# Kernel tuning notes

Measured on AMD Instinct MI355X. Metric: run time of the kernel, lower is better.

Reference implementation:

```python
import jax, jax.numpy as jnp
import numpy as np

B, C, H, W = 4, 8, 384, 384
CHANS = 18  # MLP hidden width (module default chans=18)
BAND = 32   # half-width of acquired low-frequency band


def setup_inputs() -> dict:
    key = jax.random.key(0)
    ks = jax.random.split(key, 8)
    acquired_kspace = jax.random.normal(ks[0], (B, C, H, W, 2), jnp.float32)
    acquiring_kspace = jax.random.normal(ks[1], (B, C, H, W, 2), jnp.float32)
    mid = W // 2
    am = np.zeros((B, W), np.float32)
    am[:, mid - BAND:mid + BAND] = 1.0  # acquired center band -> left/right well-defined
    acquired_mask = jnp.asarray(am)
    qm = np.zeros((B, W), np.float32)
    qm[:, ::24] = 1.0  # columns currently being acquired
    acquiring_mask = jnp.asarray(qm)
    CH = C * H
    IN = 2 * CH  # concat(acquiring_features, acquired_features)
    # MLP: Linear(IN,CHANS)+ReLU, Linear(CHANS,CHANS)+ReLU x2, Linear(CHANS,1)+Sigmoid (pools=4 layers)
    W1 = jax.random.normal(ks[2], (CHANS, IN), jnp.float32) * 0.02
    b1 = jnp.zeros((CHANS,), jnp.float32)
    W2 = jax.random.normal(ks[3], (CHANS, CHANS), jnp.float32) * 0.02
    b2 = jnp.zeros((CHANS,), jnp.float32)
    W3 = jax.random.normal(ks[4], (CHANS, CHANS), jnp.float32) * 0.02
    b3 = jnp.zeros((CHANS,), jnp.float32)
    W4 = jax.random.normal(ks[5], (1, CHANS), jnp.float32) * 0.02
    b4 = jnp.zeros((1,), jnp.float32)
    return dict(acquired_kspace=acquired_kspace, acquiring_kspace=acquiring_kspace,
                acquired_mask=acquired_mask, acquiring_mask=acquiring_mask,
                W1=W1, b1=b1, W2=W2, b2=b2, W3=W3, b3=b3, W4=W4, b4=b4)


def reference(acquired_kspace, acquiring_kspace, acquired_mask, acquiring_mask,
              W1, b1, W2, b2, W3, b3, W4, b4):
    cabs = lambda x: jnp.sqrt(jnp.sum(x * x, axis=-1))  # complex magnitude of trailing (re,im)
    # per-column flattened features, row-major over (C,H) like torch.flatten: [B, W, C*H]
    Fq = cabs(acquiring_kspace).transpose(0, 3, 1, 2).reshape(B, W, -1)
    Fa = cabs(acquired_kspace).transpose(0, 3, 1, 2).reshape(B, W, -1)
    CH = Fq.shape[-1]
    # split first linear over the concat([acquiring, acquired]) input
    Pq = Fq @ W1[:, :CH].T   # [B, W_i, CHANS]
    Pa = Fa @ W1[:, CH:].T   # [B, W_c, CHANS]
    h = jax.nn.relu(Pq[:, :, None, :] + Pa[:, None, :, :] + b1)  # [B, W_i, W_c, CHANS]
    h = jax.nn.relu(h @ W2.T + b2)
    h = jax.nn.relu(h @ W3.T + b3)
    out = jax.nn.sigmoid(h @ W4.T + b4)[..., 0]  # [B, W_i, W_c]
    # faithful left/right bounds from acquired_mask (same as torch.nonzero(...)[0][0])
    mid = W // 2
    right = mid + jnp.argmax(acquired_mask[:, mid:] < 1.0, axis=1)              # [B]
    left = jnp.argmax(acquired_mask[:, :mid][:, ::-1] < 1.0, axis=1) + 1        # [B]
    c = jnp.arange(W)
    cmask = (c[None, :] >= left[:, None]) & (c[None, :] < right[:, None])       # [B, W_c]
    denom = (right - left).astype(out.dtype)
    heat = jnp.sum(out * cmask[:, None, :].astype(out.dtype), axis=2) / denom[:, None]
    heat = jnp.where(acquiring_mask > 0, heat, jnp.zeros_like(heat))            # only nonzero acquiring cols
    return jnp.broadcast_to(heat[:, None, :], (B, H, W))  # torch.cat of h copies along dim=1
```

## Files before the change

### kernel.cpp

```cpp
#include <hip/hip_runtime.h>
#include <math.h>
#include <limits.h>

#define kB 4
#define kC 8
#define kH 384
#define kW 384
#define kCH (kC * kH)
#define kIN (2 * kCH)
#define kNC 18
#define kMID (kW / 2)

#define NCH 8
#define RPC (kCH / NCH)
#define NGRP 48
#define kN (kB * kW * kNC)

#define E18(M) M(0) M(1) M(2) M(3) M(4) M(5) M(6) M(7) M(8) M(9) M(10) M(11) M(12) M(13) M(14) M(15) M(16) M(17)
#define E12(M) M(0) M(1) M(2) M(3) M(4) M(5) M(6) M(7) M(8) M(9) M(10) M(11)

__global__ __launch_bounds__(256)
void proj_kernel(const float* __restrict__ acquired,
                 const float* __restrict__ acquiring,
                 const float* __restrict__ am,
                 const float* __restrict__ qm,
                 const float* __restrict__ W1,
                 float* __restrict__ Pq_part, float* __restrict__ Pa_part) {
    int g = blockIdx.x, chunk = blockIdx.y, b = blockIdx.z;
    int tid = threadIdx.x;
    int w0 = g * 8;
    int r0 = chunk * RPC;

    __shared__ int sL[256], sR[256];
    __shared__ float sQm[8];
    int candR = INT_MAX, candL = INT_MAX;
    for (int i = tid; i < kW - kMID; i += 256)
        if (am[b * kW + kMID + i] < 1.0f) candR = min(candR, i);
    for (int i = tid; i < kMID; i += 256)
        if (am[b * kW + (kMID - 1 - i)] < 1.0f) candL = min(candL, i);
    sL[tid] = candL; sR[tid] = candR;
    if (tid < 8) sQm[tid] = qm[b * kW + w0 + tid];
    __syncthreads();
    for (int s = 128; s > 0; s >>= 1) {
        if (tid < s) {
            sL[tid] = min(sL[tid], sL[tid + s]);
            sR[tid] = min(sR[tid], sR[tid + s]);
        }
        __syncthreads();
    }
    int left  = ((sL[0] == INT_MAX) ? 0 : sL[0]) + 1;
    int right = kMID + ((sR[0] == INT_MAX) ? 0 : sR[0]);

    bool band = (left < w0 + 8) && (right > w0);
    bool acq_any = (sQm[0] > 0.f) || (sQm[1] > 0.f) || (sQm[2] > 0.f) || (sQm[3] > 0.f) ||
                   (sQm[4] > 0.f) || (sQm[5] > 0.f) || (sQm[6] > 0.f) || (sQm[7] > 0.f);
    if (!band && !acq_any) return;

    int c8 = tid & 7, r32 = tid >> 3;
    int w = w0 + c8;
    int lane = tid & 63, wave = tid >> 6;

    __shared__ float sW[RPC][20];
    __shared__ float sRed[4][8][kNC];

    for (int pass = 0; pass < 2; ++pass) {
        bool need = (pass == 0) ? band : acq_any;
        if (!need) continue;
        const float* ks = (pass == 0) ? acquired : acquiring;
        const float* w1 = (pass == 0) ? (W1 + kCH) : W1;

        const float* colp = ks + ((size_t)(b * kCH + r0 + r32) * kW + w) * 2;
#define KLOAD(it) const float2 v##it = *reinterpret_cast<const float2*>(colp + (size_t)(it) * 32 * kW * 2);
        E12(KLOAD)
#define KMAG(it) const float f##it = sqrtf(v##it.x * v##it.x + v##it.y * v##it.y);
        E12(KMAG)

        __syncthreads();
        for (int t = tid; t < kNC * RPC; t += 256) {
            int j = t / RPC, i = t - j * RPC;
            sW[i][j] = w1[j * kIN + r0 + i];
        }
        __syncthreads();

#define PDECL(j) float a##j = 0.0f;
        E18(PDECL)

#define ROWF(it) { \
            const float* row = &sW[r32 + 32 * (it)][0]; \
            const float4 q0 = *reinterpret_cast<const float4*>(row); \
            const float4 q1 = *reinterpret_cast<const float4*>(row + 4); \
            const float4 q2 = *reinterpret_cast<const float4*>(row + 8); \
            const float4 q3 = *reinterpret_cast<const float4*>(row + 12); \
            const float2 q4 = *reinterpret_cast<const float2*>(row + 16); \
            const float f = f##it; \
            a0  = fmaf(f, q0.x, a0);  a1  = fmaf(f, q0.y, a1);  \
            a2  = fmaf(f, q0.z, a2);  a3  = fmaf(f, q0.w, a3);  \
            a4  = fmaf(f, q1.x, a4);  a5  = fmaf(f, q1.y, a5);  \
            a6  = fmaf(f, q1.z, a6);  a7  = fmaf(f, q1.w, a7);  \
            a8  = fmaf(f, q2.x, a8);  a9  = fmaf(f, q2.y, a9);  \
            a10 = fmaf(f, q2.z, a10); a11 = fmaf(f, q2.w, a11); \
            a12 = fmaf(f, q3.x, a12); a13 = fmaf(f, q3.y, a13); \
            a14 = fmaf(f, q3.z, a14); a15 = fmaf(f, q3.w, a15); \
            a16 = fmaf(f, q4.x, a16); a17 = fmaf(f, q4.y, a17); }
        E12(ROWF)

#define WRED(j) { a##j += __shfl_down(a##j, 32, 64); a##j += __shfl_down(a##j, 16, 64); \
                  a##j += __shfl_down(a##j, 8, 64); }
        E18(WRED)
        if (lane < 8) {
#define SSTORE(j) sRed[wave][lane][j] = a##j;
            E18(SSTORE)
        }
        __syncthreads();
        if (tid < 8 * kNC) {
            int c = tid / kNC, j = tid - c * kNC;
            float s = sRed[0][c][j] + sRed[1][c][j] + sRed[2][c][j] + sRed[3][c][j];
            float* Pp = (pass == 0) ? Pa_part : Pq_part;
            Pp[((size_t)chunk * kB * kW + (size_t)b * kW + (w0 + c)) * kNC + j] = s;
        }
    }
}

__global__ __launch_bounds__(256)
void reduce_kernel(const float* __restrict__ Pa_part, const float* __restrict__ Pq_part,
                   float* __restrict__ Pa, float* __restrict__ Pq) {
    int idx = blockIdx.x * 256 + threadIdx.x;
    if (idx >= 2 * kN) return;
    const float* src = (idx < kN) ? Pa_part : Pq_part;
    float* dst = (idx < kN) ? Pa : Pq;
    int n = (idx < kN) ? idx : idx - kN;
    float s = 0.0f;
#pragma unroll
    for (int c = 0; c < NCH; ++c) s += src[(size_t)c * kN + n];
    dst[n] = s;
}

__global__ __launch_bounds__(256)
void pair_kernel(const float* __restrict__ Pq, const float* __restrict__ Pa,
                 const float* __restrict__ am, const float* __restrict__ qmask,
                 const float* __restrict__ b1, const float* __restrict__ W2,
                 const float* __restrict__ b2, const float* __restrict__ W3,
                 const float* __restrict__ b3, const float* __restrict__ W4,
                 const float* __restrict__ b4, float* __restrict__ heat) {
    int wi = blockIdx.x, b = blockIdx.y, tid = threadIdx.x;
    if (!(qmask[b * kW + wi] > 0.0f)) return;

    __shared__ int sL[256], sR[256];
    int candR = INT_MAX, candL = INT_MAX;
    for (int i = tid; i < kW - kMID; i += 256)
        if (am[b * kW + kMID + i] < 1.0f) candR = min(candR, i);
    for (int i = tid; i < kMID; i += 256)
        if (am[b * kW + (kMID - 1 - i)] < 1.0f) candL = min(candL, i);
    sL[tid] = candL; sR[tid] = candR;
    __syncthreads();
    for (int s = 128; s > 0; s >>= 1) {
        if (tid < s) {
            sL[tid] = min(sL[tid], sL[tid + s]);
            sR[tid] = min(sR[tid], sR[tid + s]);
        }
        __syncthreads();
    }
    int left  = ((sL[0] == INT_MAX) ? 0 : sL[0]) + 1;
    int right = kMID + ((sR[0] == INT_MAX) ? 0 : sR[0]);
    int span = right - left;

    __shared__ float2 sW2[kNC * kNC / 2], sW3[kNC * kNC / 2];
    __shared__ float sW4[kNC], sb1[kNC], sb2[kNC], sb3[kNC], sPq[kNC];
    __shared__ float sb4s, wred[4];
    if (tid < kNC * kNC / 2) {
        sW2[tid] = reinterpret_cast<const float2*>(W2)[tid];
        sW3[tid] = reinterpret_cast<const float2*>(W3)[tid];
    }
    if (tid >= 192 && tid < 192 + kNC) {
        int j = tid - 192;
        sPq[j] = Pq[((size_t)(b * kW + wi)) * kNC + j];
        sW4[j] = W4[j]; sb1[j] = b1[j]; sb2[j] = b2[j]; sb3[j] = b3[j];
    }
    if (tid == 255) sb4s = b4[0];
    __syncthreads();

#define DOT2(S, k, v) (S[(k)*9+0].x*v##0  + S[(k)*9+0].y*v##1  + \
                       S[(k)*9+1].x*v##2  + S[(k)*9+1].y*v##3  + \
                       S[(k)*9+2].x*v##4  + S[(k)*9+2].y*v##5  + \
                       S[(k)*9+3].x*v##6  + S[(k)*9+3].y*v##7  + \
                       S[(k)*9+4].x*v##8  + S[(k)*9+4].y*v##9  + \
                       S[(k)*9+5].x*v##10 + S[(k)*9+5].y*v##11 + \
                       S[(k)*9+6].x*v##12 + S[(k)*9+6].y*v##13 + \
                       S[(k)*9+7].x*v##14 + S[(k)*9+7].y*v##15 + \
                       S[(k)*9+8].x*v##16 + S[(k)*9+8].y*v##17)

    float ssum = 0.0f;
    for (int wc = left + tid; wc < right; wc += 256) {
        const float* pa = Pa + (size_t)(b * kW + wc) * kNC;
#define L1(j) float x##j = fmaxf(sPq[j] + sb1[j] + pa[j], 0.0f);
        E18(L1)
        asm volatile("" ::: "memory");
#define L2(k) float y##k = fmaxf(sb2[k] + DOT2(sW2, k, x), 0.0f);
        E18(L2)
        asm volatile("" ::: "memory");
#define L3(k) float z##k = fmaxf(sb3[k] + DOT2(sW3, k, y), 0.0f);
        E18(L3)
        asm volatile("" ::: "memory");
        float t = sb4s +
            (sW4[0]*z0 + sW4[1]*z1 + sW4[2]*z2 + sW4[3]*z3 + sW4[4]*z4 + sW4[5]*z5 +
             sW4[6]*z6 + sW4[7]*z7 + sW4[8]*z8 + sW4[9]*z9 + sW4[10]*z10 + sW4[11]*z11 +
             sW4[12]*z12 + sW4[13]*z13 + sW4[14]*z14 + sW4[15]*z15 + sW4[16]*z16 + sW4[17]*z17);
        ssum += 1.0f / (1.0f + expf(-t));
    }

    ssum += __shfl_down(ssum, 32, 64); ssum += __shfl_down(ssum, 16, 64);
    ssum += __shfl_down(ssum,  8, 64); ssum += __shfl_down(ssum,  4, 64);
    ssum += __shfl_down(ssum,  2, 64); ssum += __shfl_down(ssum,  1, 64);
    int wave = tid >> 6, lane = tid & 63;
    if (lane == 0) wred[wave] = ssum;
    __syncthreads();
    if (tid == 0)
        heat[b * kW + wi] = (wred[0] + wred[1] + wred[2] + wred[3]) / (float)span;
}

__global__ __launch_bounds__(256)
void out_kernel(const float* __restrict__ heat, const float* __restrict__ qm,
                float* __restrict__ out) {
    int idx = blockIdx.x * 256 + threadIdx.x;
    if (idx >= kB * kH * kW) return;
    int w = idx % kW;
    int b = idx / (kH * kW);
    out[idx] = (qm[b * kW + w] > 0.0f) ? heat[b * kW + w] : 0.0f;
}

extern "C" void kernel_launch(void* const* d_in, const int* in_sizes, int n_in,
                              void* d_out, int out_size, void* d_ws, size_t ws_size,
                              hipStream_t stream) {
    const float* acquired       = (const float*)d_in[0];
    const float* acquiring      = (const float*)d_in[1];
    const float* acquired_mask  = (const float*)d_in[2];
    const float* acquiring_mask = (const float*)d_in[3];
    const float* W1 = (const float*)d_in[4];
    const float* b1 = (const float*)d_in[5];
    const float* W2 = (const float*)d_in[6];
    const float* b2 = (const float*)d_in[7];
    const float* W3 = (const float*)d_in[8];
    const float* b3 = (const float*)d_in[9];
    const float* W4 = (const float*)d_in[10];
    const float* b4 = (const float*)d_in[11];
    float* out = (float*)d_out;

    float* Pa_part = (float*)d_ws;
    float* Pq_part = Pa_part + (size_t)NCH * kN;
    float* Pa      = Pq_part + (size_t)NCH * kN;
    float* Pq      = Pa + kN;
    float* heat    = Pq + kN;

    proj_kernel<<<dim3(NGRP, NCH, kB), 256, 0, stream>>>(
        acquired, acquiring, acquired_mask, acquiring_mask, W1, Pq_part, Pa_part);
    reduce_kernel<<<(2 * kN + 255) / 256, 256, 0, stream>>>(Pa_part, Pq_part, Pa, Pq);
    pair_kernel<<<dim3(kW, kB), 256, 0, stream>>>(
        Pq, Pa, acquired_mask, acquiring_mask,
        b1, W2, b2, W3, b3, W4, b4, heat);
    int n = kB * kH * kW;
    out_kernel<<<(n + 255) / 256, 256, 0, stream>>>(heat, acquiring_mask, out);
}
```

Before: 149.8 us.

## Fuse reduce and output kernels into proj/pair and split passes across blocks

Cuts the pipeline from four kernel launches to two. The chunk-partial reduction moves into pair_kernel, which stages the summed Pa band into shared memory. The output broadcast is folded in: zeros are written by proj_kernel blocks and the heat columns by pair_kernel. proj_kernel now runs each pass (acquired vs acquiring) in its own block for more parallelism, and mask-bound detection uses wave ballots instead of a shared-memory min reduction. The trade-off is redundant partial sums across pair blocks, plus a scattered column-strided output write and one more early-exit check per block.

```diff
diff --git a/kernel.cpp b/kernel.cpp
--- a/kernel.cpp
+++ b/kernel.cpp
@@ -19,164 +19,166 @@
 #define E18(M) M(0) M(1) M(2) M(3) M(4) M(5) M(6) M(7) M(8) M(9) M(10) M(11) M(12) M(13) M(14) M(15) M(16) M(17)
 #define E12(M) M(0) M(1) M(2) M(3) M(4) M(5) M(6) M(7) M(8) M(9) M(10) M(11)
 
+__device__ __forceinline__ void mask_bounds(const float* __restrict__ amb,
+                                            int lane, int* left, int* right) {
+    unsigned long long mR0 = __ballot(amb[kMID + lane] < 1.0f);
+    unsigned long long mR1 = __ballot(amb[kMID + 64 + lane] < 1.0f);
+    unsigned long long mR2 = __ballot(amb[kMID + 128 + lane] < 1.0f);
+    unsigned long long mL0 = __ballot(amb[kMID - 1 - lane] < 1.0f);
+    unsigned long long mL1 = __ballot(amb[kMID - 65 - lane] < 1.0f);
+    unsigned long long mL2 = __ballot(amb[kMID - 129 - lane] < 1.0f);
+    int candR = mR0 ? __builtin_ctzll(mR0)
+              : (mR1 ? 64 + __builtin_ctzll(mR1)
+              : (mR2 ? 128 + __builtin_ctzll(mR2) : 0));
+    int candL = mL0 ? __builtin_ctzll(mL0)
+              : (mL1 ? 64 + __builtin_ctzll(mL1)
+              : (mL2 ? 128 + __builtin_ctzll(mL2) : 0));
+    *left  = candL + 1;
+    *right = kMID + candR;
+}
+
 __global__ __launch_bounds__(256)
 void proj_kernel(const float* __restrict__ acquired,
                  const float* __restrict__ acquiring,
                  const float* __restrict__ am,
                  const float* __restrict__ qm,
                  const float* __restrict__ W1,
-                 float* __restrict__ Pq_part, float* __restrict__ Pa_part) {
-    int g = blockIdx.x, chunk = blockIdx.y, b = blockIdx.z;
+                 float* __restrict__ Pq_part, float* __restrict__ Pa_part,
+                 float* __restrict__ out) {
+    int g = blockIdx.x;
+    int chunk = blockIdx.y & (NCH - 1);
+    int pass = blockIdx.y >> 3;
+    int b = blockIdx.z;
     int tid = threadIdx.x;
     int w0 = g * 8;
     int r0 = chunk * RPC;
 
-    __shared__ int sL[256], sR[256];
-    __shared__ float sQm[8];
-    int candR = INT_MAX, candL = INT_MAX;
-    for (int i = tid; i < kW - kMID; i += 256)
-        if (am[b * kW + kMID + i] < 1.0f) candR = min(candR, i);
-    for (int i = tid; i < kMID; i += 256)
-        if (am[b * kW + (kMID - 1 - i)] < 1.0f) candL = min(candL, i);
-    sL[tid] = candL; sR[tid] = candR;
-    if (tid < 8) sQm[tid] = qm[b * kW + w0 + tid];
-    __syncthreads();
-    for (int s = 128; s > 0; s >>= 1) {
-        if (tid < s) {
-            sL[tid] = min(sL[tid], sL[tid + s]);
-            sR[tid] = min(sR[tid], sR[tid + s]);
+    {
+        int flatB = (blockIdx.z * gridDim.y + blockIdx.y) * gridDim.x + blockIdx.x;
+        int gid = flatB * 256 + tid;
+        if (gid < kB * kH * kW) {
+            int w = gid % kW;
+            int ob = gid / (kH * kW);
+            if (!(qm[ob * kW + w] > 0.0f)) out[gid] = 0.0f;
         }
-        __syncthreads();
-    }
-    int left  = ((sL[0] == INT_MAX) ? 0 : sL[0]) + 1;
-    int right = kMID + ((sR[0] == INT_MAX) ? 0 : sR[0]);
-
-    bool band = (left < w0 + 8) && (right > w0);
-    bool acq_any = (sQm[0] > 0.f) || (sQm[1] > 0.f) || (sQm[2] > 0.f) || (sQm[3] > 0.f) ||
-                   (sQm[4] > 0.f) || (sQm[5] > 0.f) || (sQm[6] > 0.f) || (sQm[7] > 0.f);
-    if (!band && !acq_any) return;
+    }
+
+    int lane = tid & 63;
+    bool need;
+    if (pass == 0) {
+        int left, right;
+        mask_bounds(am + b * kW, lane, &left, &right);
+        need = (left < w0 + 8) && (right > w0);
+    } else {
+        bool q = qm[b * kW + w0 + (lane & 7)] > 0.0f;
+        need = (__ballot(q) != 0ull);
+    }
+    if (!need) return;
+
+    const float* ks = (pass == 0) ? acquired : acquiring;
+    const float* w1 = (pass == 0) ? (W1 + kCH) : W1;
 
     int c8 = tid & 7, r32 = tid >> 3;
     int w = w0 + c8;
-    int lane = tid & 63, wave = tid >> 6;
+    int wave = tid >> 6;
 
     __shared__ float sW[RPC][20];
     __shared__ float sRed[4][8][kNC];
 
-    for (int pass = 0; pass < 2; ++pass) {
-        bool need = (pass == 0) ? band : acq_any;
-        if (!need) continue;
-        const float* ks = (pass == 0) ? acquired : acquiring;
-        const float* w1 = (pass == 0) ? (W1 + kCH) : W1;
-
-        const float* colp = ks + ((size_t)(b * kCH + r0 + r32) * kW + w) * 2;
+    const float* colp = ks + ((size_t)(b * kCH + r0 + r32) * kW + w) * 2;
 #define KLOAD(it) const float2 v##it = *reinterpret_cast<const float2*>(colp + (size_t)(it) * 32 * kW * 2);
-        E12(KLOAD)
+    E12(KLOAD)
+
+    for (int t = tid; t < kNC * RPC; t += 256) {
+        int j = t / RPC, i = t - j * RPC;
+        sW[i][j] = w1[j * kIN + r0 + i];
+    }
+    __syncthreads();
+
 #define KMAG(it) const float f##it = sqrtf(v##it.x * v##it.x + v##it.y * v##it.y);
-        E12(KMAG)
-
-        __syncthreads();
-        for (int t = tid; t < kNC * RPC; t += 256) {
-            int j = t / RPC, i = t - j * RPC;
-            sW[i][j] = w1[j * kIN + r0 + i];
-        }
-        __syncthreads();
+    E12(KMAG)
 
 #define PDECL(j) float a##j = 0.0f;
-        E18(PDECL)
+    E18(PDECL)
 
 #define ROWF(it) { \
-            const float* row = &sW[r32 + 32 * (it)][0]; \
-            const float4 q0 = *reinterpret_cast<const float4*>(row); \
-            const float4 q1 = *reinterpret_cast<const float4*>(row + 4); \
-            const float4 q2 = *reinterpret_cast<const float4*>(row + 8); \
-            const float4 q3 = *reinterpret_cast<const float4*>(row + 12); \
-            const float2 q4 = *reinterpret_cast<const float2*>(row + 16); \
-            const float f = f##it; \
-            a0  = fmaf(f, q0.x, a0);  a1  = fmaf(f, q0.y, a1);  \
-            a2  = fmaf(f, q0.z, a2);  a3  = fmaf(f, q0.w, a3);  \
-            a4  = fmaf(f, q1.x, a4);  a5  = fmaf(f, q1.y, a5);  \
-            a6  = fmaf(f, q1.z, a6);  a7  = fmaf(f, q1.w, a7);  \
-            a8  = fmaf(f, q2.x, a8);  a9  = fmaf(f, q2.y, a9);  \
-            a10 = fmaf(f, q2.z, a10); a11 = fmaf(f, q2.w, a11); \
-            a12 = fmaf(f, q3.x, a12); a13 = fmaf(f, q3.y, a13); \
-            a14 = fmaf(f, q3.z, a14); a15 = fmaf(f, q3.w, a15); \
-            a16 = fmaf(f, q4.x, a16); a17 = fmaf(f, q4.y, a17); }
-        E12(ROWF)
+        const float* row = &sW[r32 + 32 * (it)][0]; \
+        const float4 q0 = *reinterpret_cast<const float4*>(row); \
+        const float4 q1 = *reinterpret_cast<const float4*>(row + 4); \
+        const float4 q2 = *reinterpret_cast<const float4*>(row + 8); \
+        const float4 q3 = *reinterpret_cast<const float4*>(row + 12); \
+        const float2 q4 = *reinterpret_cast<const float2*>(row + 16); \
+        const float f = f##it; \
+        a0  = fmaf(f, q0.x, a0);  a1  = fmaf(f, q0.y, a1);  \
+        a2  = fmaf(f, q0.z, a2);  a3  = fmaf(f, q0.w, a3);  \
+        a4  = fmaf(f, q1.x, a4);  a5  = fmaf(f, q1.y, a5);  \
+        a6  = fmaf(f, q1.z, a6);  a7  = fmaf(f, q1.w, a7);  \
+        a8  = fmaf(f, q2.x, a8);  a9  = fmaf(f, q2.y, a9);  \
+        a10 = fmaf(f, q2.z, a10); a11 = fmaf(f, q2.w, a11); \
+        a12 = fmaf(f, q3.x, a12); a13 = fmaf(f, q3.y, a13); \
+        a14 = fmaf(f, q3.z, a14); a15 = fmaf(f, q3.w, a15); \
+        a16 = fmaf(f, q4.x, a16); a17 = fmaf(f, q4.y, a17); }
+    E12(ROWF)
 
 #define WRED(j) { a##j += __shfl_down(a##j, 32, 64); a##j += __shfl_down(a##j, 16, 64); \
                   a##j += __shfl_down(a##j, 8, 64); }
-        E18(WRED)
-        if (lane < 8) {
+    E18(WRED)
+    if (lane < 8) {
 #define SSTORE(j) sRed[wave][lane][j] = a##j;
-            E18(SSTORE)
-        }
-        __syncthreads();
-        if (tid < 8 * kNC) {
-            int c = tid / kNC, j = tid - c * kNC;
-            float s = sRed[0][c][j] + sRed[1][c][j] + sRed[2][c][j] + sRed[3][c][j];
-            float* Pp = (pass == 0) ? Pa_part : Pq_part;
-            Pp[((size_t)chunk * kB * kW + (size_t)b * kW + (w0 + c)) * kNC + j] = s;
-        }
+        E18(SSTORE)
+    }
+    __syncthreads();
+    if (tid < 8 * kNC) {
+        int c = tid / kNC, j = tid - c * kNC;
+        float s = sRed[0][c][j] + sRed[1][c][j] + sRed[2][c][j] + sRed[3][c][j];
+        float* Pp = (pass == 0) ? Pa_part : Pq_part;
+        Pp[((size_t)chunk * kB * kW + (size_t)b * kW + (w0 + c)) * kNC + j] = s;
     }
 }
 
 __global__ __launch_bounds__(256)
-void reduce_kernel(const float* __restrict__ Pa_part, const float* __restrict__ Pq_part,
-                   float* __restrict__ Pa, float* __restrict__ Pq) {
-    int idx = blockIdx.x * 256 + threadIdx.x;
-    if (idx >= 2 * kN) return;
-    const float* src = (idx < kN) ? Pa_part : Pq_part;
-    float* dst = (idx < kN) ? Pa : Pq;
-    int n = (idx < kN) ? idx : idx - kN;
-    float s = 0.0f;
-#pragma unroll
-    for (int c = 0; c < NCH; ++c) s += src[(size_t)c * kN + n];
-    dst[n] = s;
-}
-
-__global__ __launch_bounds__(256)
-void pair_kernel(const float* __restrict__ Pq, const float* __restrict__ Pa,
+void pair_kernel(const float* __restrict__ Pq_part, const float* __restrict__ Pa_part,
                  const float* __restrict__ am, const float* __restrict__ qmask,
                  const float* __restrict__ b1, const float* __restrict__ W2,
                  const float* __restrict__ b2, const float* __restrict__ W3,
                  const float* __restrict__ b3, const float* __restrict__ W4,
-                 const float* __restrict__ b4, float* __restrict__ heat) {
+                 const float* __restrict__ b4, float* __restrict__ out) {
     int wi = blockIdx.x, b = blockIdx.y, tid = threadIdx.x;
     if (!(qmask[b * kW + wi] > 0.0f)) return;
 
-    __shared__ int sL[256], sR[256];
-    int candR = INT_MAX, candL = INT_MAX;
-    for (int i = tid; i < kW - kMID; i += 256)
-        if (am[b * kW + kMID + i] < 1.0f) candR = min(candR, i);
-    for (int i = tid; i < kMID; i += 256)
-        if (am[b * kW + (kMID - 1 - i)] < 1.0f) candL = min(candL, i);
-    sL[tid] = candL; sR[tid] = candR;
-    __syncthreads();
-    for (int s = 128; s > 0; s >>= 1) {
-        if (tid < s) {
-            sL[tid] = min(sL[tid], sL[tid + s]);
-            sR[tid] = min(sR[tid], sR[tid + s]);
-        }
-        __syncthreads();
-    }
-    int left  = ((sL[0] == INT_MAX) ? 0 : sL[0]) + 1;
-    int right = kMID + ((sR[0] == INT_MAX) ? 0 : sR[0]);
+    int lane = tid & 63, wave = tid >> 6;
+    int left, right;
+    mask_bounds(am + b * kW, lane, &left, &right);
     int span = right - left;
 
+    __shared__ float sPa[kW][19];
     __shared__ float2 sW2[kNC * kNC / 2], sW3[kNC * kNC / 2];
     __shared__ float sW4[kNC], sb1[kNC], sb2[kNC], sb3[kNC], sPq[kNC];
-    __shared__ float sb4s, wred[4];
+    __shared__ float sb4s, wred[4], sHeat;
+
     if (tid < kNC * kNC / 2) {
         sW2[tid] = reinterpret_cast<const float2*>(W2)[tid];
         sW3[tid] = reinterpret_cast<const float2*>(W3)[tid];
     }
     if (tid >= 192 && tid < 192 + kNC) {
         int j = tid - 192;
-        sPq[j] = Pq[((size_t)(b * kW + wi)) * kNC + j];
+        float s = 0.0f;
+#pragma unroll
+        for (int c = 0; c < NCH; ++c)
+            s += Pq_part[((size_t)c * kB * kW + (size_t)b * kW + wi) * kNC + j];
+        sPq[j] = s;
         sW4[j] = W4[j]; sb1[j] = b1[j]; sb2[j] = b2[j]; sb3[j] = b3[j];
     }
     if (tid == 255) sb4s = b4[0];
+
+    for (int t = tid; t < span * kNC; t += 256) {
+        int k = t / kNC, j = t - k * kNC;
+        float s = 0.0f;
+#pragma unroll
+        for (int c = 0; c < NCH; ++c)
+            s += Pa_part[((size_t)c * kB * kW + (size_t)b * kW + (left + k)) * kNC + j];
+        sPa[k][j] = s;
+    }
     __syncthreads();
 
 #define DOT2(S, k, v) (S[(k)*9+0].x*v##0  + S[(k)*9+0].y*v##1  + \
@@ -190,8 +192,8 @@
                        S[(k)*9+8].x*v##16 + S[(k)*9+8].y*v##17)
 
     float ssum = 0.0f;
-    for (int wc = left + tid; wc < right; wc += 256) {
-        const float* pa = Pa + (size_t)(b * kW + wc) * kNC;
+    for (int k = tid; k < span; k += 256) {
+        const float* pa = &sPa[k][0];
 #define L1(j) float x##j = fmaxf(sPq[j] + sb1[j] + pa[j], 0.0f);
         E18(L1)
         asm volatile("" ::: "memory");
@@ -211,21 +213,15 @@
     ssum += __shfl_down(ssum, 32, 64); ssum += __shfl_down(ssum, 16, 64);
     ssum += __shfl_down(ssum,  8, 64); ssum += __shfl_down(ssum,  4, 64);
     ssum += __shfl_down(ssum,  2, 64); ssum += __shfl_down(ssum,  1, 64);
-    int wave = tid >> 6, lane = tid & 63;
     if (lane == 0) wred[wave] = ssum;
     __syncthreads();
     if (tid == 0)
-        heat[b * kW + wi] = (wred[0] + wred[1] + wred[2] + wred[3]) / (float)span;
-}
-
-__global__ __launch_bounds__(256)
-void out_kernel(const float* __restrict__ heat, const float* __restrict__ qm,
-                float* __restrict__ out) {
-    int idx = blockIdx.x * 256 + threadIdx.x;
-    if (idx >= kB * kH * kW) return;
-    int w = idx % kW;
-    int b = idx / (kH * kW);
-    out[idx] = (qm[b * kW + w] > 0.0f) ? heat[b * kW + w] : 0.0f;
+        sHeat = (wred[0] + wred[1] + wred[2] + wred[3]) / (float)span;
+    __syncthreads();
+
+    float hv = sHeat;
+    for (int h = tid; h < kH; h += 256)
+        out[((size_t)b * kH + h) * kW + wi] = hv;
 }
 
 extern "C" void kernel_launch(void* const* d_in, const int* in_sizes, int n_in,
@@ -247,16 +243,10 @@
 
     float* Pa_part = (float*)d_ws;
     float* Pq_part = Pa_part + (size_t)NCH * kN;
-    float* Pa      = Pq_part + (size_t)NCH * kN;
-    float* Pq      = Pa + kN;
-    float* heat    = Pq + kN;
-
-    proj_kernel<<<dim3(NGRP, NCH, kB), 256, 0, stream>>>(
-        acquired, acquiring, acquired_mask, acquiring_mask, W1, Pq_part, Pa_part);
-    reduce_kernel<<<(2 * kN + 255) / 256, 256, 0, stream>>>(Pa_part, Pq_part, Pa, Pq);
+
+    proj_kernel<<<dim3(NGRP, 2 * NCH, kB), 256, 0, stream>>>(
+        acquired, acquiring, acquired_mask, acquiring_mask, W1, Pq_part, Pa_part, out);
     pair_kernel<<<dim3(kW, kB), 256, 0, stream>>>(
-        Pq, Pa, acquired_mask, acquiring_mask,
-        b1, W2, b2, W3, b3, W4, b4, heat);
-    int n = kB * kH * kW;
-    out_kernel<<<(n + 255) / 256, 256, 0, stream>>>(heat, acquiring_mask, out);
-}
+        Pq_part, Pa_part, acquired_mask, acquiring_mask,
+        b1, W2, b2, W3, b3, W4, b4, out);
+}
```

New measurement: 145.8 us. 1.03x faster.
